# Kernel tuning notes

Hardware: AMD Instinct MI355X
Metric: run time of the kernel (lower is better)

The kernel has to match this reference:

```python
import jax, jax.numpy as jnp
import numpy as np

B, S, D, A = 64, 2048, 512, 512


def setup_inputs() -> dict:
    key = jax.random.key(0)
    ks = jax.random.split(key, 6)
    return {
        "input": jax.random.normal(ks[0], (B, D), dtype=jnp.float32),
        "context": jax.random.normal(ks[1], (B, S, D), dtype=jnp.float32),
        "Wh": jax.random.uniform(ks[2], (D, A), dtype=jnp.float32, minval=-0.1, maxval=0.1),
        "Ws": jax.random.uniform(ks[3], (D, A), dtype=jnp.float32, minval=-0.1, maxval=0.1),
        "b_attn": jax.random.uniform(ks[4], (A,), dtype=jnp.float32, minval=-0.1, maxval=0.1),
        "va": jax.random.uniform(ks[5], (A,), dtype=jnp.float32, minval=-0.1, maxval=0.1),
    }


def reference(input, context, Wh, Ws, b_attn, va):
    # _concat score: tanh(ht@Wh + context@Ws + b) @ va  -> [B, S]
    ht_proj = input @ Wh                      # [B, A]
    ctx_proj = jnp.einsum("bsd,da->bsa", context, Ws)  # [B, S, A]
    concat = jnp.tanh(ht_proj[:, None, :] + ctx_proj + b_attn)  # [B, S, A]
    attn = jnp.einsum("bsa,a->bs", concat, va)  # [B, S]
    # padding mask: positions whose mean feature is exactly 0
    context_mask = jnp.mean(context, axis=-1) == 0  # [B, S]
    attn = jnp.where(context_mask, -jnp.inf, attn)
    attn_dist = jax.nn.softmax(attn, axis=1)  # [B, S]
    attn_context = jnp.einsum("bsd,bs->bd", context, attn_dist)  # [B, D]
    return attn_context, attn_dist
```

## Files before the change

kernel.cpp:

```cpp
#include <hip/hip_runtime.h>
#include <hip/hip_bf16.h>
#include <math.h>

#define B_ 64
#define S_ 2048
#define D_ 512
#define A_ 512

typedef __attribute__((ext_vector_type(8))) short short8;
typedef __attribute__((ext_vector_type(4))) short short4b;
typedef __attribute__((ext_vector_type(4))) float f32x4;

__device__ __forceinline__ short bf16b(float f) {
    __hip_bfloat16 h = __float2bfloat16(f);
    union { __hip_bfloat16 h; short s; } u; u.h = h;
    return u.s;
}

__device__ __forceinline__ float tanh_fast(float x) {
    float e = __expf(2.0f * x);
    return 1.0f - 2.0f / (e + 1.0f);
}

__device__ __forceinline__ void llds16(const void* g, void* l) {
    __builtin_amdgcn_global_load_lds(
        (const __attribute__((address_space(1))) unsigned int*)g,
        (__attribute__((address_space(3))) unsigned int*)l, 16, 0, 0);
}

__global__ __launch_bounds__(256) void k_prep(const float* __restrict__ input,
                                              const float* __restrict__ Wh,
                                              const float* __restrict__ b_attn,
                                              const float* __restrict__ Ws,
                                              float* __restrict__ htWb,
                                              short* __restrict__ WsT) {
    const int t = threadIdx.x;
    if (blockIdx.x < 64) {
        __shared__ float xin[512];
        const int b = blockIdx.x;
        xin[t] = input[b * D_ + t];
        xin[t + 256] = input[b * D_ + t + 256];
        __syncthreads();
        float a0 = 0.f, a1 = 0.f;
#pragma unroll 8
        for (int d = 0; d < D_; ++d) {
            const float xv = xin[d];
            a0 += xv * Wh[d * A_ + t];
            a1 += xv * Wh[d * A_ + t + 256];
        }
        htWb[b * A_ + t] = a0 + b_attn[t];
        htWb[b * A_ + t + 256] = a1 + b_attn[t + 256];
    } else {
        const int blk = blockIdx.x - 64;
        const int bx = blk & 7, by = blk >> 3;
        const int r0 = by * 64, c0 = bx * 64;
        __shared__ short tile[64][72];
        const int row = t >> 4, col4 = (t & 15) * 4;
#pragma unroll
        for (int i = 0; i < 4; ++i) {
            const float4 v = *(const float4*)&Ws[(r0 + row + i * 16) * A_ + c0 + col4];
            tile[col4 + 0][row + i * 16] = bf16b(v.x);
            tile[col4 + 1][row + i * 16] = bf16b(v.y);
            tile[col4 + 2][row + i * 16] = bf16b(v.z);
            tile[col4 + 3][row + i * 16] = bf16b(v.w);
        }
        __syncthreads();
#pragma unroll
        for (int i = 0; i < 4; ++i) {
            const int arow = row + i * 16;
            short4b o;
            o.x = tile[arow][col4 + 0];
            o.y = tile[arow][col4 + 1];
            o.z = tile[arow][col4 + 2];
            o.w = tile[arow][col4 + 3];
            *(short4b*)&WsT[(c0 + arow) * D_ + r0 + col4] = o;
        }
    }
}

__global__ __launch_bounds__(512, 2)
void k_score3(const float* __restrict__ ctx, const short* __restrict__ WsT,
              const float* __restrict__ htWb, const float* __restrict__ va,
              float* __restrict__ scores) {
    __shared__ __align__(16) short Bb[2][512 * 32];
    __shared__ __align__(16) short Ab[128 * 32];
    __shared__ float hv_s[512];
    __shared__ float va_s[512];
    __shared__ float scores_s[128];
    __shared__ float rowsum_s[128];

    const int tid = threadIdx.x;
    const int w = tid >> 6, lane = tid & 63;
    const int wm = w >> 2, wn = w & 3;
    const int blk = blockIdx.x;
    const int b = blk >> 4;
    const int s0 = (blk & 15) * 128;
    const long rowbase = (long)b * S_ + s0;

    hv_s[tid] = htWb[b * A_ + tid];
    va_s[tid] = va[tid];
    if (tid < 128) scores_s[tid] = 0.f;

    const int arow = tid >> 2, aq = tid & 3;
    const float* aSrc = ctx + (rowbase + arow) * (long)D_;
    float rowsum_acc = 0.f;

    f32x4 acc[4][8];
#pragma unroll
    for (int i = 0; i < 4; ++i)
#pragma unroll
        for (int j = 0; j < 8; ++j)
#pragma unroll
            for (int e = 0; e < 4; ++e) acc[i][j][e] = 0.f;

#define STAGE_B(buf, kt)                                                      \
    {                                                                         \
        _Pragma("unroll") for (int j = 0; j < 4; ++j) {                       \
            const int a = (w * 4 + j) * 16 + (lane >> 2);                     \
            const int c = lane & 3;                                           \
            const int csw = c ^ ((a >> 1) & 3);                               \
            llds16(WsT + a * D_ + (kt) * 32 + csw * 8,                        \
                   (void*)&Bb[buf][(w * 4 + j) * 512]);                       \
        }                                                                     \
    }

#define STAGE_A_WRITE(v0, v1)                                                 \
    {                                                                         \
        rowsum_acc += (v0)[0] + (v0)[1] + (v0)[2] + (v0)[3];                  \
        rowsum_acc += (v1)[0] + (v1)[1] + (v1)[2] + (v1)[3];                  \
        short4b o0, o1;                                                       \
        o0.x = bf16b((v0)[0]); o0.y = bf16b((v0)[1]);                         \
        o0.z = bf16b((v0)[2]); o0.w = bf16b((v0)[3]);                         \
        o1.x = bf16b((v1)[0]); o1.y = bf16b((v1)[1]);                         \
        o1.z = bf16b((v1)[2]); o1.w = bf16b((v1)[3]);                         \
        const int sw = (arow >> 1) & 3;                                       \
        const int c0g = (aq >> 1), c1g = 2 + (aq >> 1), sub = aq & 1;         \
        *(short4b*)((char*)Ab + arow * 64 + ((c0g ^ sw) * 16) + sub * 8) = o0; \
        *(short4b*)((char*)Ab + arow * 64 + ((c1g ^ sw) * 16) + sub * 8) = o1; \
    }

    {
        const f32x4 v0 = *(const f32x4*)(aSrc + aq * 4);
        const f32x4 v1 = *(const f32x4*)(aSrc + aq * 4 + 16);
        STAGE_B(0, 0);
        STAGE_A_WRITE(v0, v1);
    }
    __syncthreads();

    for (int kt = 0; kt < 16; ++kt) {
        const int cur = kt & 1;
        f32x4 nv0, nv1;
        if (kt < 15) {
            const float* p0 = aSrc + (kt + 1) * 32 + aq * 4;
            asm volatile("global_load_dwordx4 %0, %1, off" : "=v"(nv0) : "v"(p0));
            asm volatile("global_load_dwordx4 %0, %1, off" : "=v"(nv1) : "v"(p0 + 16));
            __builtin_amdgcn_sched_barrier(0);
            STAGE_B(cur ^ 1, kt + 1);
            __builtin_amdgcn_sched_barrier(0);
        }
        __builtin_amdgcn_s_setprio(1);
        {
            short8 af[4];
#pragma unroll
            for (int mf = 0; mf < 4; ++mf) {
                const int r = wm * 64 + mf * 16 + (lane & 15);
                const int c = lane >> 4;
                const int csw = c ^ ((r >> 1) & 3);
                af[mf] = *(const short8*)((const char*)Ab + r * 64 + csw * 16);
            }
#pragma unroll
            for (int nf = 0; nf < 8; ++nf) {
                const int a = wn * 128 + nf * 16 + (lane & 15);
                const int c = lane >> 4;
                const int csw = c ^ ((a >> 1) & 3);
                const short8 bf =
                    *(const short8*)((const char*)&Bb[cur][0] + a * 64 + csw * 16);
#pragma unroll
                for (int mf = 0; mf < 4; ++mf)
                    acc[mf][nf] = __builtin_amdgcn_mfma_f32_16x16x32_bf16(
                        af[mf], bf, acc[mf][nf], 0, 0, 0);
            }
        }
        __builtin_amdgcn_s_setprio(0);
        asm volatile("s_waitcnt lgkmcnt(0)" ::: "memory");
        __builtin_amdgcn_sched_barrier(0);
        __builtin_amdgcn_s_barrier();
        if (kt < 15) {
            asm volatile("s_waitcnt vmcnt(4)" ::: "memory");
            __builtin_amdgcn_sched_barrier(0);
            STAGE_A_WRITE(nv0, nv1);
        }
        __syncthreads();
    }

    rowsum_acc += __shfl_xor(rowsum_acc, 1);
    rowsum_acc += __shfl_xor(rowsum_acc, 2);
    if ((tid & 3) == 0) rowsum_s[arow] = rowsum_acc;

    float hv[8], vv[8];
#pragma unroll
    for (int nf = 0; nf < 8; ++nf) {
        const int col = wn * 128 + nf * 16 + (lane & 15);
        hv[nf] = hv_s[col];
        vv[nf] = va_s[col];
    }
#pragma unroll
    for (int mf = 0; mf < 4; ++mf) {
#pragma unroll
        for (int e = 0; e < 4; ++e) {
            float p = 0.f;
#pragma unroll
            for (int nf = 0; nf < 8; ++nf)
                p += vv[nf] * tanh_fast(hv[nf] + acc[mf][nf][e]);
            p += __shfl_xor(p, 1);
            p += __shfl_xor(p, 2);
            p += __shfl_xor(p, 4);
            p += __shfl_xor(p, 8);
            if ((lane & 15) == 0) {
                const int row = wm * 64 + mf * 16 + (lane >> 4) * 4 + e;
                atomicAdd(&scores_s[row], p);
            }
        }
    }
    __syncthreads();

    if (tid < 128) {
        float sc = scores_s[tid];
        if (rowsum_s[tid] == 0.0f) sc = -__builtin_inff();
        scores[rowbase + tid] = sc;
    }
}

__global__ __launch_bounds__(256) void k_softmax(float* __restrict__ dist) {
    const int b = blockIdx.x, t = threadIdx.x;
    float* p = dist + b * S_;
    float v[8];
    float m = -__builtin_inff();
#pragma unroll
    for (int i = 0; i < 8; ++i) {
        v[i] = p[t + i * 256];
        m = fmaxf(m, v[i]);
    }
#pragma unroll
    for (int mask = 1; mask < 64; mask <<= 1) m = fmaxf(m, __shfl_xor(m, mask));
    __shared__ float redm[4], reds[4];
    if ((t & 63) == 0) redm[t >> 6] = m;
    __syncthreads();
    m = fmaxf(fmaxf(redm[0], redm[1]), fmaxf(redm[2], redm[3]));
    float sum = 0.f;
#pragma unroll
    for (int i = 0; i < 8; ++i) {
        v[i] = __expf(v[i] - m);
        sum += v[i];
    }
#pragma unroll
    for (int mask = 1; mask < 64; mask <<= 1) sum += __shfl_xor(sum, mask);
    if ((t & 63) == 0) reds[t >> 6] = sum;
    __syncthreads();
    sum = reds[0] + reds[1] + reds[2] + reds[3];
    const float inv = 1.0f / sum;
#pragma unroll
    for (int i = 0; i < 8; ++i) p[t + i * 256] = v[i] * inv;
}

__global__ __launch_bounds__(256) void k_wsum(const float* __restrict__ ctx,
                                              const float* __restrict__ dist,
                                              float* __restrict__ partial) {
    const int ch = blockIdx.x, b = blockIdx.y;
    const int t = threadIdx.x;
    const int half = t >> 7;
    const int td = (t & 127) * 4;
    __shared__ float ps[128];
    __shared__ f32x4 red[128];
    if (t < 128) ps[t] = dist[b * S_ + ch * 128 + t];
    __syncthreads();
    const float* cbase = ctx + ((long)b * S_ + ch * 128 + half * 64) * D_ + td;
    f32x4 a = {0.f, 0.f, 0.f, 0.f};
#pragma unroll 4
    for (int r = 0; r < 64; ++r) {
        const f32x4 cv = *(const f32x4*)(cbase + (long)r * D_);
        const float pw = ps[half * 64 + r];
        a[0] += pw * cv[0];
        a[1] += pw * cv[1];
        a[2] += pw * cv[2];
        a[3] += pw * cv[3];
    }
    if (half == 1) red[t & 127] = a;
    __syncthreads();
    if (half == 0) {
        const f32x4 o = red[t];
        a[0] += o[0]; a[1] += o[1]; a[2] += o[2]; a[3] += o[3];
        *(f32x4*)&partial[((b * 16 + ch) * D_) + td] = a;
    }
}

__global__ __launch_bounds__(128) void k_reduce(const float* __restrict__ partial,
                                                float* __restrict__ out) {
    const int b = blockIdx.x, t = threadIdx.x;
    float ax = 0.f, ay = 0.f, az = 0.f, aw = 0.f;
#pragma unroll
    for (int j = 0; j < 16; ++j) {
        const float4 v = *(const float4*)&partial[((b * 16 + j) * D_) + t * 4];
        ax += v.x; ay += v.y; az += v.z; aw += v.w;
    }
    float4 o; o.x = ax; o.y = ay; o.z = az; o.w = aw;
    *(float4*)&out[b * D_ + t * 4] = o;
}

extern "C" void kernel_launch(void* const* d_in, const int* in_sizes, int n_in,
                              void* d_out, int out_size, void* d_ws, size_t ws_size,
                              hipStream_t stream) {
    (void)in_sizes; (void)n_in; (void)out_size; (void)ws_size;
    const float* input  = (const float*)d_in[0];
    const float* ctx    = (const float*)d_in[1];
    const float* Wh     = (const float*)d_in[2];
    const float* Ws     = (const float*)d_in[3];
    const float* b_attn = (const float*)d_in[4];
    const float* va     = (const float*)d_in[5];

    float* out = (float*)d_out;
    float* attn_ctx  = out;
    float* attn_dist = out + B_ * D_;

    char* ws = (char*)d_ws;
    float* htWb    = (float*)ws;
    short* WsT     = (short*)(ws + 131072);
    float* partial = (float*)(ws + 131072 + 524288);

    k_prep<<<128, 256, 0, stream>>>(input, Wh, b_attn, Ws, htWb, WsT);
    k_score3<<<1024, 512, 0, stream>>>(ctx, WsT, htWb, va, attn_dist);
    k_softmax<<<64, 256, 0, stream>>>(attn_dist);
    k_wsum<<<dim3(16, 64), 256, 0, stream>>>(ctx, attn_dist, partial);
    k_reduce<<<64, 128, 0, stream>>>(partial, attn_ctx);
}
```

Measured before the change: 516.2 us.

## Pre-swizzle Ws tiles and deepen B-operand prefetch to four LDS buffers

The prep kernel now writes the transposed bf16 Ws in the exact per-k-tile swizzled order the score kernel uses. Each B tile then becomes one contiguous 16-byte-per-lane global-to-LDS copy. The score kernel keeps four B buffers and prefetches three k-tiles ahead. It changes the A load mapping to two row-halves per thread and replaces the per-iteration __syncthreads with explicit waitcnt plus s_barrier pairs. The weighted-sum loop's unroll is raised from 4 to 8. The larger B ring (about 128KB of LDS) likely leaves room for only one 512-thread block per CU instead of two, which may cost latency hiding.

```diff
diff --git a/kernel.cpp b/kernel.cpp
--- a/kernel.cpp
+++ b/kernel.cpp
@@ -10,6 +10,8 @@
 typedef __attribute__((ext_vector_type(8))) short short8;
 typedef __attribute__((ext_vector_type(4))) short short4b;
 typedef __attribute__((ext_vector_type(4))) float f32x4;
+
+#define SB() __builtin_amdgcn_sched_barrier(0)
 
 __device__ __forceinline__ short bf16b(float f) {
     __hip_bfloat16 h = __float2bfloat16(f);
@@ -33,7 +35,7 @@
                                               const float* __restrict__ b_attn,
                                               const float* __restrict__ Ws,
                                               float* __restrict__ htWb,
-                                              short* __restrict__ WsT) {
+                                              short* __restrict__ staged) {
     const int t = threadIdx.x;
     if (blockIdx.x < 64) {
         __shared__ float xin[512];
@@ -65,24 +67,29 @@
             tile[col4 + 3][row + i * 16] = bf16b(v.w);
         }
         __syncthreads();
+        const int k0 = r0 + col4;
+        const int kt = k0 >> 5;
+        const int csw = (k0 >> 3) & 3;
 #pragma unroll
         for (int i = 0; i < 4; ++i) {
-            const int arow = row + i * 16;
+            const int arel = row + i * 16;
+            const int a = c0 + arel;
             short4b o;
-            o.x = tile[arow][col4 + 0];
-            o.y = tile[arow][col4 + 1];
-            o.z = tile[arow][col4 + 2];
-            o.w = tile[arow][col4 + 3];
-            *(short4b*)&WsT[(c0 + arow) * D_ + r0 + col4] = o;
+            o.x = tile[arel][col4 + 0];
+            o.y = tile[arel][col4 + 1];
+            o.z = tile[arel][col4 + 2];
+            o.w = tile[arel][col4 + 3];
+            const int slot = (a & 15) * 4 + (csw ^ ((a >> 1) & 3));
+            *(short4b*)&staged[kt * 16384 + (a >> 4) * 512 + slot * 8 + (k0 & 7)] = o;
         }
     }
 }
 
 __global__ __launch_bounds__(512, 2)
-void k_score3(const float* __restrict__ ctx, const short* __restrict__ WsT,
+void k_score4(const float* __restrict__ ctx, const short* __restrict__ staged,
               const float* __restrict__ htWb, const float* __restrict__ va,
               float* __restrict__ scores) {
-    __shared__ __align__(16) short Bb[2][512 * 32];
+    __shared__ __align__(16) short Bb[4][512 * 32];
     __shared__ __align__(16) short Ab[128 * 32];
     __shared__ float hv_s[512];
     __shared__ float va_s[512];
@@ -101,9 +108,11 @@
     va_s[tid] = va[tid];
     if (tid < 128) scores_s[tid] = 0.f;
 
-    const int arow = tid >> 2, aq = tid & 3;
-    const float* aSrc = ctx + (rowbase + arow) * (long)D_;
-    float rowsum_acc = 0.f;
+    const int row0 = tid >> 3, q = tid & 7;
+    const int row1 = row0 + 64;
+    const float* aSrc0 = ctx + (rowbase + row0) * (long)D_ + q * 4;
+    const float* aSrc1 = aSrc0 + 64 * D_;
+    float rs0 = 0.f, rs1 = 0.f;
 
     f32x4 acc[4][8];
 #pragma unroll
@@ -113,50 +122,57 @@
 #pragma unroll
             for (int e = 0; e < 4; ++e) acc[i][j][e] = 0.f;
 
-#define STAGE_B(buf, kt)                                                      \
+#define STAGE_B4(buf, kt_)                                                    \
     {                                                                         \
         _Pragma("unroll") for (int j = 0; j < 4; ++j) {                       \
-            const int a = (w * 4 + j) * 16 + (lane >> 2);                     \
-            const int c = lane & 3;                                           \
-            const int csw = c ^ ((a >> 1) & 3);                               \
-            llds16(WsT + a * D_ + (kt) * 32 + csw * 8,                        \
-                   (void*)&Bb[buf][(w * 4 + j) * 512]);                       \
+            const int g = w * 4 + j;                                          \
+            llds16(staged + (kt_) * 16384 + g * 512 + lane * 8,               \
+                   (void*)&Bb[buf][g * 512]);                                 \
         }                                                                     \
     }
 
 #define STAGE_A_WRITE(v0, v1)                                                 \
     {                                                                         \
-        rowsum_acc += (v0)[0] + (v0)[1] + (v0)[2] + (v0)[3];                  \
-        rowsum_acc += (v1)[0] + (v1)[1] + (v1)[2] + (v1)[3];                  \
+        rs0 += (v0)[0] + (v0)[1] + (v0)[2] + (v0)[3];                         \
+        rs1 += (v1)[0] + (v1)[1] + (v1)[2] + (v1)[3];                         \
         short4b o0, o1;                                                       \
         o0.x = bf16b((v0)[0]); o0.y = bf16b((v0)[1]);                         \
         o0.z = bf16b((v0)[2]); o0.w = bf16b((v0)[3]);                         \
         o1.x = bf16b((v1)[0]); o1.y = bf16b((v1)[1]);                         \
         o1.z = bf16b((v1)[2]); o1.w = bf16b((v1)[3]);                         \
-        const int sw = (arow >> 1) & 3;                                       \
-        const int c0g = (aq >> 1), c1g = 2 + (aq >> 1), sub = aq & 1;         \
-        *(short4b*)((char*)Ab + arow * 64 + ((c0g ^ sw) * 16) + sub * 8) = o0; \
-        *(short4b*)((char*)Ab + arow * 64 + ((c1g ^ sw) * 16) + sub * 8) = o1; \
+        const int cq = q >> 1, sub = q & 1;                                   \
+        *(short4b*)((char*)Ab + row0 * 64 + ((cq ^ ((row0 >> 1) & 3)) * 16) + sub * 8) = o0; \
+        *(short4b*)((char*)Ab + row1 * 64 + ((cq ^ ((row1 >> 1) & 3)) * 16) + sub * 8) = o1; \
     }
 
     {
-        const f32x4 v0 = *(const f32x4*)(aSrc + aq * 4);
-        const f32x4 v1 = *(const f32x4*)(aSrc + aq * 4 + 16);
-        STAGE_B(0, 0);
+        const f32x4 v0 = *(const f32x4*)(aSrc0);
+        const f32x4 v1 = *(const f32x4*)(aSrc1);
         STAGE_A_WRITE(v0, v1);
     }
-    __syncthreads();
+    STAGE_B4(0, 0);
+    STAGE_B4(1, 1);
+    STAGE_B4(2, 2);
+    asm volatile("s_waitcnt vmcnt(8)" ::: "memory");
+    SB();
+    asm volatile("s_waitcnt lgkmcnt(0)" ::: "memory");
+    SB();
+    __builtin_amdgcn_s_barrier();
+    SB();
 
     for (int kt = 0; kt < 16; ++kt) {
-        const int cur = kt & 1;
+        const int cur = kt & 3;
         f32x4 nv0, nv1;
         if (kt < 15) {
-            const float* p0 = aSrc + (kt + 1) * 32 + aq * 4;
+            const float* p0 = aSrc0 + (kt + 1) * 32;
+            const float* p1 = aSrc1 + (kt + 1) * 32;
             asm volatile("global_load_dwordx4 %0, %1, off" : "=v"(nv0) : "v"(p0));
-            asm volatile("global_load_dwordx4 %0, %1, off" : "=v"(nv1) : "v"(p0 + 16));
-            __builtin_amdgcn_sched_barrier(0);
-            STAGE_B(cur ^ 1, kt + 1);
-            __builtin_amdgcn_sched_barrier(0);
+            asm volatile("global_load_dwordx4 %0, %1, off" : "=v"(nv1) : "v"(p1));
+            SB();
+        }
+        if (kt < 13) {
+            STAGE_B4((kt + 3) & 3, kt + 3);
+            SB();
         }
         __builtin_amdgcn_s_setprio(1);
         {
@@ -183,19 +199,30 @@
         }
         __builtin_amdgcn_s_setprio(0);
         asm volatile("s_waitcnt lgkmcnt(0)" ::: "memory");
-        __builtin_amdgcn_sched_barrier(0);
+        SB();
         __builtin_amdgcn_s_barrier();
+        SB();
         if (kt < 15) {
-            asm volatile("s_waitcnt vmcnt(4)" ::: "memory");
-            __builtin_amdgcn_sched_barrier(0);
+            if (kt < 13) {
+                asm volatile("s_waitcnt vmcnt(4)" ::: "memory");
+            } else {
+                asm volatile("s_waitcnt vmcnt(0)" ::: "memory");
+            }
+            SB();
             STAGE_A_WRITE(nv0, nv1);
-        }
-        __syncthreads();
-    }
-
-    rowsum_acc += __shfl_xor(rowsum_acc, 1);
-    rowsum_acc += __shfl_xor(rowsum_acc, 2);
-    if ((tid & 3) == 0) rowsum_s[arow] = rowsum_acc;
+            asm volatile("s_waitcnt lgkmcnt(0)" ::: "memory");
+            SB();
+            __builtin_amdgcn_s_barrier();
+            SB();
+        }
+    }
+
+    rs0 += __shfl_xor(rs0, 1); rs0 += __shfl_xor(rs0, 2); rs0 += __shfl_xor(rs0, 4);
+    rs1 += __shfl_xor(rs1, 1); rs1 += __shfl_xor(rs1, 2); rs1 += __shfl_xor(rs1, 4);
+    if ((tid & 7) == 0) {
+        rowsum_s[row0] = rs0;
+        rowsum_s[row1] = rs1;
+    }
 
     float hv[8], vv[8];
 #pragma unroll
@@ -276,7 +303,7 @@
     __syncthreads();
     const float* cbase = ctx + ((long)b * S_ + ch * 128 + half * 64) * D_ + td;
     f32x4 a = {0.f, 0.f, 0.f, 0.f};
-#pragma unroll 4
+#pragma unroll 8
     for (int r = 0; r < 64; ++r) {
         const f32x4 cv = *(const f32x4*)(cbase + (long)r * D_);
         const float pw = ps[half * 64 + r];
@@ -324,11 +351,11 @@
 
     char* ws = (char*)d_ws;
     float* htWb    = (float*)ws;
-    short* WsT     = (short*)(ws + 131072);
+    short* staged  = (short*)(ws + 131072);
     float* partial = (float*)(ws + 131072 + 524288);
 
-    k_prep<<<128, 256, 0, stream>>>(input, Wh, b_attn, Ws, htWb, WsT);
-    k_score3<<<1024, 512, 0, stream>>>(ctx, WsT, htWb, va, attn_dist);
+    k_prep<<<128, 256, 0, stream>>>(input, Wh, b_attn, Ws, htWb, staged);
+    k_score4<<<1024, 512, 0, stream>>>(ctx, staged, htWb, va, attn_dist);
     k_softmax<<<64, 256, 0, stream>>>(attn_dist);
     k_wsum<<<dim3(16, 64), 256, 0, stream>>>(ctx, attn_dist, partial);
     k_reduce<<<64, 128, 0, stream>>>(partial, attn_ctx);
```

After: 527.4 us. +2.2%, slower.
